# Kernel optimization log

Hardware: AMD Instinct MI355X
Metric: run time of the kernel (lower is better)

Reference implementation:

```python
import jax, jax.numpy as jnp
import numpy as np

B, L, C, H, K = 4096, 64, 7, 32, 2  # batch, series length, input ch, hidden ch, RK4 substeps per knot


def _linear_params(k, out_d, in_d):
    bound = 1.0 / np.sqrt(in_d)
    kw, kb = jax.random.split(k)
    W = jax.random.uniform(kw, (out_d, in_d), minval=-bound, maxval=bound, dtype=jnp.float32)
    b = jax.random.uniform(kb, (out_d,), minval=-bound, maxval=bound, dtype=jnp.float32)
    return W, b


def setup_inputs() -> dict:
    key = jax.random.key(0)
    ks = jax.random.split(key, 6)
    cde_src = jax.random.normal(ks[0], (B, L, C), dtype=jnp.float32)
    W_init, b_init = _linear_params(ks[1], H, C)          # initial: Linear(C, H)
    Wf1, bf1 = _linear_params(ks[2], 32, H)               # func.linear1: Linear(H, 32)
    Wf2, bf2 = _linear_params(ks[3], C * H, 32)           # func.linear2: Linear(32, C*H)
    Wo1, bo1 = _linear_params(ks[4], 16, H)               # linear1: Linear(H, 16)
    Wo2, bo2 = _linear_params(ks[5], 3, 16)               # linear2: Linear(16, 3)
    return {"cde_src": cde_src, "W_init": W_init, "b_init": b_init,
            "Wf1": Wf1, "bf1": bf1, "Wf2": Wf2, "bf2": bf2,
            "Wo1": Wo1, "bo1": bo1, "Wo2": Wo2, "bo2": bo2}


def reference(cde_src, W_init, b_init, Wf1, bf1, Wf2, bf2, Wo1, bo1, Wo2, bo2):
    x = cde_src  # (B, L, C); uniform times t = 0..L-1 (torchcde default), so dt = 1
    # Hermite cubic coefficients with backward differences (torchcde), dt = 1:
    diffs = x[:, 1:] - x[:, :-1]                       # (B, L-1, C) backward differences
    d = jnp.concatenate([diffs[:, :1], diffs], axis=1)  # derivative at each knot
    m0, m1 = d[:, :-1], d[:, 1:]
    cb = m0                                            # 'b' coeff (= dX/dt at left knot)
    two_c = 2.0 * (3.0 * diffs - 2.0 * m0 - m1)        # (B, L-1, C)
    three_d = 3.0 * (-2.0 * diffs + m0 + m1)           # (B, L-1, C)

    z0 = x[:, 0] @ W_init.T + b_init                   # initial(X(t0))  -> (B, H)

    def dXdt(t):
        idx = jnp.clip(jnp.floor(t), 0, L - 2).astype(jnp.int32)
        f = t - idx.astype(t.dtype)
        return cb[:, idx] + (two_c[:, idx] + three_d[:, idx] * f) * f  # (B, C)

    def vf(t, z):
        h1 = jax.nn.softplus(z @ Wf1.T + bf1)                    # (B, 32)
        g = jnp.tanh(h1 @ Wf2.T + bf2).reshape(z.shape[0], H, C)  # (B, H, C)
        return jnp.einsum('bhc,bc->bh', g, dXdt(t))

    h = 1.0 / K
    times = jnp.arange((L - 1) * K, dtype=jnp.float32) * h

    def step(z, t):
        k1 = vf(t, z)
        k2 = vf(t + 0.5 * h, z + (0.5 * h) * k1)
        k3 = vf(t + 0.5 * h, z + (0.5 * h) * k2)
        k4 = vf(t + h, z + h * k3)
        return z + (h / 6.0) * (k1 + 2.0 * k2 + 2.0 * k3 + k4), None

    zT, _ = jax.lax.scan(step, z0, times)  # z at final time (== zT[:, 1] in torch)
    out = jax.nn.softplus(zT @ Wo1.T + bo1) @ Wo2.T + bo2  # (B, 3)
    return out
```

## Files before the change

### kernel.cpp

```cpp
#include <hip/hip_runtime.h>
#include <hip/hip_bf16.h>
#include <stdint.h>

typedef __bf16 bf16_t;
typedef __bf16 bf16x8 __attribute__((ext_vector_type(8)));
typedef float f32x4 __attribute__((ext_vector_type(4)));

#define LOG2E 1.44269504088896340736f
#define LN2 0.69314718055994530942f

__device__ __forceinline__ float fast_exp2(float x) { return __builtin_amdgcn_exp2f(x); }
__device__ __forceinline__ float fast_log2(float x) { return __builtin_amdgcn_logf(x); }
__device__ __forceinline__ float fast_rcp(float x) { return __builtin_amdgcn_rcpf(x); }

__device__ __forceinline__ float softplus_t(float t) {
    float sp = LN2 * fast_log2(1.0f + fast_exp2(t));
    return (t > 28.9f) ? t * LN2 : sp;
}
__device__ __forceinline__ float tanh_t(float t) {
    float e = fast_exp2(t);
    return 1.0f - 2.0f * fast_rcp(1.0f + e);
}

__device__ __forceinline__ uint32_t cvt_bf16(float a) {
    uint32_t r;
    asm("v_cvt_pk_bf16_f32 %0, %1, %2" : "=v"(r) : "v"(a), "v"(a));
    return r;
}
__device__ __forceinline__ void store_hl(float v, uint16_t* ph, uint16_t* pl) {
    uint32_t h = cvt_bf16(v);
    float hf = __builtin_bit_cast(float, h << 16);
    uint32_t lo = cvt_bf16(v - hf);
    *ph = (uint16_t)h;
    *pl = (uint16_t)lo;
}

__device__ __forceinline__ float swz16(float v) {
    int r = __builtin_amdgcn_ds_swizzle(__builtin_bit_cast(int, v), 0x401F);
    return __builtin_bit_cast(float, r);
}

__global__ __launch_bounds__(512, 2) void cde_kernel(
    const float* __restrict__ x,
    const float* __restrict__ Wi,
    const float* __restrict__ bi,
    const float* __restrict__ W1,
    const float* __restrict__ b1,
    const float* __restrict__ W2,
    const float* __restrict__ b2,
    const float* __restrict__ Wo1,
    const float* __restrict__ bo1,
    const float* __restrict__ Wo2,
    const float* __restrict__ bo2,
    float* __restrict__ out)
{
    __shared__ float diffs[16][441];
    __shared__ alignas(16) float dxA[16][12];
    __shared__ alignas(16) float dxB[16][12];
    __shared__ alignas(16) uint16_t zth[16][40], ztl[16][40];
    __shared__ alignas(16) uint16_t hth[16][40], htl[16][40];
    __shared__ float zfin[16][32];
    __shared__ float wo1t[32][16];
    __shared__ float ubuf[16][16];

    const int tid = threadIdx.x;
    const int l = tid & 63;
    const int w = tid >> 6;
    const int r0 = blockIdx.x * 16;

    const int ar = l & 15;
    const int q = l >> 4;

    const int T1 = w & 1;
    const int rw = w >> 1;
    const int i1 = 16 * T1 + 4 * q + rw;

    const int h2a = 4 * w + (q >> 1);
    const int h2b = h2a + 2;

    const int bdx = 2 * w + (l >> 5);
    const int cdx = l & 31;
    const bool dxact = cdx < 7;

    bf16x8 a1h, a1l;
    {
        const float* p = &W1[(16 * T1 + ar) * 32 + 8 * q];
#pragma unroll
        for (int j = 0; j < 8; ++j) {
            float v = p[j] * LOG2E;
            bf16_t hh = (bf16_t)v;
            a1h[j] = hh;
            a1l[j] = (bf16_t)(v - (float)hh);
        }
    }
    f32x4 b1v;
#pragma unroll
    for (int r = 0; r < 4; ++r) b1v[r] = b1[16 * T1 + 4 * q + r] * LOG2E;

    bf16x8 a2h[2], a2l[2];
    f32x4 b2v[2];
#pragma unroll
    for (int t = 0; t < 2; ++t) {
        const int T = 2 * w + t;
        const int hh2 = 2 * T + (ar >> 3);
        const int cc = ar & 7;
        if (cc < 7) {
            const float* p = &W2[(hh2 * 7 + cc) * 32 + 8 * q];
#pragma unroll
            for (int j = 0; j < 8; ++j) {
                float v = p[j] * (2.0f * LOG2E);
                bf16_t hv = (bf16_t)v;
                a2h[t][j] = hv;
                a2l[t][j] = (bf16_t)(v - (float)hv);
            }
        } else {
#pragma unroll
            for (int j = 0; j < 8; ++j) { a2h[t][j] = (bf16_t)0.0f; a2l[t][j] = (bf16_t)0.0f; }
        }
#pragma unroll
        for (int r = 0; r < 4; ++r) {
            int c = 4 * (q & 1) + r;
            int hq = 2 * T + (q >> 1);
            b2v[t][r] = (c < 7) ? b2[hq * 7 + c] * (2.0f * LOG2E) : 0.0f;
        }
    }

    const bf16x8* pZh = (const bf16x8*)&zth[ar][8 * q];
    const bf16x8* pZl = (const bf16x8*)&ztl[ar][8 * q];
    const bf16x8* pHh = (const bf16x8*)&hth[ar][8 * q];
    const bf16x8* pHl = (const bf16x8*)&htl[ar][8 * q];
    const f32x4* pDxA = (const f32x4*)&dxA[ar][4 * (q & 1)];
    const f32x4* pDxB = (const f32x4*)&dxB[ar][4 * (q & 1)];
    uint16_t* pWh = &hth[ar][i1];
    uint16_t* pWl = &htl[ar][i1];
    uint16_t* pZah = &zth[ar][h2a];
    uint16_t* pZal = &ztl[ar][h2a];
    uint16_t* pZbh = &zth[ar][h2b];
    uint16_t* pZbl = &ztl[ar][h2b];

    for (int e = tid; e < 16 * 441; e += 512) {
        int r = e / 441, rem = e - r * 441;
        const float* px = &x[(size_t)(r0 + r) * 448];
        diffs[r][rem] = px[rem + 7] - px[rem];
    }
    if (tid < 16) { dxA[tid][7] = 0.0f; dxB[tid][7] = 0.0f; }
    if (dxact) {
        const float* px = &x[(size_t)(r0 + bdx) * 448];
        dxA[bdx][cdx] = px[cdx + 7] - px[cdx];
    }
    float zb0, zb1, ka0 = 0.0f, ka1 = 0.0f;
    {
        const float* px = &x[(size_t)(r0 + ar) * 448];
        float a0 = bi[h2a], a1 = bi[h2b];
#pragma unroll
        for (int c = 0; c < 7; ++c) {
            a0 += px[c] * Wi[h2a * 7 + c];
            a1 += px[c] * Wi[h2b * 7 + c];
        }
        zb0 = a0; zb1 = a1;
        store_hl(zb0, pZah, pZal);
        store_hl(zb1, pZbh, pZbl);
    }
    __syncthreads();

    const f32x4 zero4 = {0.0f, 0.0f, 0.0f, 0.0f};

    for (int k = 0; k < 126; ++k) {
#pragma unroll
        for (int s = 0; s < 4; ++s) {
            {
                bf16x8 bzh = *pZh;
                bf16x8 bzl = *pZl;
                f32x4 m1 = __builtin_amdgcn_mfma_f32_16x16x32_bf16(a1h, bzh, b1v, 0, 0, 0);
                f32x4 m2 = __builtin_amdgcn_mfma_f32_16x16x32_bf16(a1h, bzl, zero4, 0, 0, 0);
                f32x4 m3 = __builtin_amdgcn_mfma_f32_16x16x32_bf16(a1l, bzh, zero4, 0, 0, 0);
                float X;
                if (rw == 0)      X = m1[0] + m2[0] + m3[0];
                else if (rw == 1) X = m1[1] + m2[1] + m3[1];
                else if (rw == 2) X = m1[2] + m2[2] + m3[2];
                else              X = m1[3] + m2[3] + m3[3];
                store_hl(softplus_t(X), pWh, pWl);
            }
            if ((s == 0 || s == 1) && dxact) {
                int m = 2 * k + 1 + s;
                int i = m >> 2; if (i > 62) i = 62;
                float f = 0.25f * (float)(m - 4 * i);
                float D = diffs[bdx][i * 7 + cdx];
                float a = diffs[bdx][(i > 0 ? i - 1 : 0) * 7 + cdx];
                float val = a + (D - a) * (f * (4.0f - 3.0f * f));
                if (s == 0) dxB[bdx][cdx] = val;
                else        dxA[bdx][cdx] = val;
            }
            __syncthreads();

            {
                bf16x8 bhh = *pHh;
                bf16x8 bhl = *pHl;
                f32x4 dxv = (s == 0 || s == 3) ? *pDxA : *pDxB;
                float ks0, ks1;
#pragma unroll
                for (int t = 0; t < 2; ++t) {
                    f32x4 n1 = __builtin_amdgcn_mfma_f32_16x16x32_bf16(a2h[t], bhh, b2v[t], 0, 0, 0);
                    f32x4 n2 = __builtin_amdgcn_mfma_f32_16x16x32_bf16(a2h[t], bhl, zero4, 0, 0, 0);
                    f32x4 n3 = __builtin_amdgcn_mfma_f32_16x16x32_bf16(a2l[t], bhh, zero4, 0, 0, 0);
                    float pk = 0.0f;
#pragma unroll
                    for (int r = 0; r < 4; ++r)
                        pk += tanh_t(n1[r] + n2[r] + n3[r]) * dxv[r];
                    float kst = pk + swz16(pk);
                    if (t == 0) ks0 = kst; else ks1 = kst;
                }
                float zs0, zs1;
                if (s == 0) {
                    ka0 = ks0; ka1 = ks1;
                    zs0 = zb0 + 0.25f * ks0; zs1 = zb1 + 0.25f * ks1;
                } else if (s == 1) {
                    ka0 += 2.0f * ks0; ka1 += 2.0f * ks1;
                    zs0 = zb0 + 0.25f * ks0; zs1 = zb1 + 0.25f * ks1;
                } else if (s == 2) {
                    ka0 += 2.0f * ks0; ka1 += 2.0f * ks1;
                    zs0 = zb0 + 0.5f * ks0; zs1 = zb1 + 0.5f * ks1;
                } else {
                    zb0 += (1.0f / 12.0f) * (ka0 + ks0);
                    zb1 += (1.0f / 12.0f) * (ka1 + ks1);
                    zs0 = zb0; zs1 = zb1;
                }
                store_hl(zs0, pZah, pZal);
                store_hl(zs1, pZbh, pZbl);
            }
            __syncthreads();
        }
    }

    zfin[ar][h2a] = zb0;
    zfin[ar][h2b] = zb1;
    {
        int hh = tid >> 4, jj = tid & 15;
        wo1t[hh][jj] = Wo1[jj * 32 + hh];
    }
    __syncthreads();
    if (tid < 256) {
        int r = tid >> 4, jj = tid & 15;
        float acc = bo1[jj];
#pragma unroll
        for (int hh = 0; hh < 32; ++hh) acc += zfin[r][hh] * wo1t[hh][jj];
        ubuf[r][jj] = softplus_t(acc * LOG2E);
    }
    __syncthreads();
    if (tid < 48) {
        int r = tid / 3, o = tid - (tid / 3) * 3;
        float acc = bo2[o];
#pragma unroll
        for (int j = 0; j < 16; ++j) acc += ubuf[r][j] * Wo2[o * 16 + j];
        out[(size_t)(r0 + r) * 3 + o] = acc;
    }
}

extern "C" void kernel_launch(void* const* d_in, const int* in_sizes, int n_in,
                              void* d_out, int out_size, void* d_ws, size_t ws_size,
                              hipStream_t stream) {
    (void)in_sizes; (void)n_in; (void)d_ws; (void)ws_size; (void)out_size;
    const float* x   = (const float*)d_in[0];
    const float* Wi  = (const float*)d_in[1];
    const float* bi  = (const float*)d_in[2];
    const float* W1  = (const float*)d_in[3];
    const float* b1  = (const float*)d_in[4];
    const float* W2  = (const float*)d_in[5];
    const float* b2  = (const float*)d_in[6];
    const float* Wo1 = (const float*)d_in[7];
    const float* bo1 = (const float*)d_in[8];
    const float* Wo2 = (const float*)d_in[9];
    const float* bo2 = (const float*)d_in[10];
    cde_kernel<<<dim3(256), dim3(512), 0, stream>>>(x, Wi, bi, W1, b1, W2, b2,
                                                    Wo1, bo1, Wo2, bo2, (float*)d_out);
}
```

Baseline: 446.0 us.

## Halve rows per block to 8 with 4 waves and repartition MFMA work

Each block now handles 8 batch rows with 256 threads (4 waves), launching 512 blocks instead of 256 blocks of 512 threads. Each wave computes four second-layer MFMA tiles instead of two, and the 16-wide MFMA B operand is padded with zero rows for the unused half. The shared-memory z/h staging is re-laid out per wave-quadrant with packed bf16 hi/lo conversion of two values at once. The intent is more blocks across CUs and cheaper barriers with fewer waves, at the cost of wasting half of each MFMA on padding rows.

```diff
diff --git a/kernel.cpp b/kernel.cpp
--- a/kernel.cpp
+++ b/kernel.cpp
@@ -22,17 +22,10 @@
     return 1.0f - 2.0f * fast_rcp(1.0f + e);
 }
 
-__device__ __forceinline__ uint32_t cvt_bf16(float a) {
+__device__ __forceinline__ uint32_t cvt_pk(float a, float b) {
     uint32_t r;
-    asm("v_cvt_pk_bf16_f32 %0, %1, %2" : "=v"(r) : "v"(a), "v"(a));
+    asm("v_cvt_pk_bf16_f32 %0, %1, %2" : "=v"(r) : "v"(a), "v"(b));
     return r;
-}
-__device__ __forceinline__ void store_hl(float v, uint16_t* ph, uint16_t* pl) {
-    uint32_t h = cvt_bf16(v);
-    float hf = __builtin_bit_cast(float, h << 16);
-    uint32_t lo = cvt_bf16(v - hf);
-    *ph = (uint16_t)h;
-    *pl = (uint16_t)lo;
 }
 
 __device__ __forceinline__ float swz16(float v) {
@@ -40,7 +33,7 @@
     return __builtin_bit_cast(float, r);
 }
 
-__global__ __launch_bounds__(512, 2) void cde_kernel(
+__global__ __launch_bounds__(256, 2) void cde_kernel(
     const float* __restrict__ x,
     const float* __restrict__ Wi,
     const float* __restrict__ bi,
@@ -54,28 +47,28 @@
     const float* __restrict__ bo2,
     float* __restrict__ out)
 {
-    __shared__ float diffs[16][441];
+    __shared__ float diffs[8][441];
     __shared__ alignas(16) float dxA[16][12];
     __shared__ alignas(16) float dxB[16][12];
-    __shared__ alignas(16) uint16_t zth[16][40], ztl[16][40];
-    __shared__ alignas(16) uint16_t hth[16][40], htl[16][40];
+    __shared__ alignas(16) uint16_t zhS[4][16][8], zlS[4][16][8];
+    __shared__ alignas(16) uint16_t hhS[4][16][8], hlS[4][16][8];
     __shared__ float zfin[16][32];
     __shared__ float wo1t[32][16];
-    __shared__ float ubuf[16][16];
+    __shared__ float ubuf[8][16];
 
     const int tid = threadIdx.x;
     const int l = tid & 63;
     const int w = tid >> 6;
-    const int r0 = blockIdx.x * 16;
+    const int r0 = blockIdx.x * 8;
 
     const int ar = l & 15;
     const int q = l >> 4;
-
-    const int T1 = w & 1;
-    const int rw = w >> 1;
-    const int i1 = 16 * T1 + 4 * q + rw;
-
-    const int h2a = 4 * w + (q >> 1);
+    const int qlo = q & 1, qhi = q >> 1;
+    const bool brow = ar < 8;
+
+    const int T1 = w & 1, rp = w >> 1;
+
+    const int h2a = 8 * w + 4 * qlo + qhi;
     const int h2b = h2a + 2;
 
     const int bdx = 2 * w + (l >> 5);
@@ -97,15 +90,15 @@
 #pragma unroll
     for (int r = 0; r < 4; ++r) b1v[r] = b1[16 * T1 + 4 * q + r] * LOG2E;
 
-    bf16x8 a2h[2], a2l[2];
-    f32x4 b2v[2];
-#pragma unroll
-    for (int t = 0; t < 2; ++t) {
-        const int T = 2 * w + t;
-        const int hh2 = 2 * T + (ar >> 3);
+    bf16x8 a2h[4], a2l[4];
+    f32x4 b2v[4];
+#pragma unroll
+    for (int t = 0; t < 4; ++t) {
+        const int T = 4 * w + t;
+        const int hrow = 2 * T + (ar >> 3);
         const int cc = ar & 7;
         if (cc < 7) {
-            const float* p = &W2[(hh2 * 7 + cc) * 32 + 8 * q];
+            const float* p = &W2[(hrow * 7 + cc) * 32 + 8 * q];
 #pragma unroll
             for (int j = 0; j < 8; ++j) {
                 float v = p[j] * (2.0f * LOG2E);
@@ -119,37 +112,41 @@
         }
 #pragma unroll
         for (int r = 0; r < 4; ++r) {
-            int c = 4 * (q & 1) + r;
-            int hq = 2 * T + (q >> 1);
+            int c = 4 * qlo + r;
+            int hq = 2 * T + qhi;
             b2v[t][r] = (c < 7) ? b2[hq * 7 + c] * (2.0f * LOG2E) : 0.0f;
         }
     }
 
-    const bf16x8* pZh = (const bf16x8*)&zth[ar][8 * q];
-    const bf16x8* pZl = (const bf16x8*)&ztl[ar][8 * q];
-    const bf16x8* pHh = (const bf16x8*)&hth[ar][8 * q];
-    const bf16x8* pHl = (const bf16x8*)&htl[ar][8 * q];
-    const f32x4* pDxA = (const f32x4*)&dxA[ar][4 * (q & 1)];
-    const f32x4* pDxB = (const f32x4*)&dxB[ar][4 * (q & 1)];
-    uint16_t* pWh = &hth[ar][i1];
-    uint16_t* pWl = &htl[ar][i1];
-    uint16_t* pZah = &zth[ar][h2a];
-    uint16_t* pZal = &ztl[ar][h2a];
-    uint16_t* pZbh = &zth[ar][h2b];
-    uint16_t* pZbl = &ztl[ar][h2b];
-
-    for (int e = tid; e < 16 * 441; e += 512) {
+    const bf16x8* pZh = (const bf16x8*)&zhS[q][ar][0];
+    const bf16x8* pZl = (const bf16x8*)&zlS[q][ar][0];
+    const bf16x8* pHh = (const bf16x8*)&hhS[q][ar][0];
+    const bf16x8* pHl = (const bf16x8*)&hlS[q][ar][0];
+    const f32x4* pDxA = (const f32x4*)&dxA[ar][4 * qlo];
+    const f32x4* pDxB = (const f32x4*)&dxB[ar][4 * qlo];
+    uint32_t* pWh = (uint32_t*)&hhS[2 * T1 + qhi][ar][4 * qlo + 2 * rp];
+    uint32_t* pWl = (uint32_t*)&hlS[2 * T1 + qhi][ar][4 * qlo + 2 * rp];
+    uint16_t* pZ0h = &zhS[w][ar][4 * qlo + qhi];
+    uint16_t* pZ0l = &zlS[w][ar][4 * qlo + qhi];
+    uint16_t* pZ1h = &zhS[w][ar][4 * qlo + qhi + 2];
+    uint16_t* pZ1l = &zlS[w][ar][4 * qlo + qhi + 2];
+
+    ((uint32_t*)zhS)[tid] = 0;
+    ((uint32_t*)zlS)[tid] = 0;
+    ((uint32_t*)hhS)[tid] = 0;
+    ((uint32_t*)hlS)[tid] = 0;
+    if (tid < 192) { ((float*)dxA)[tid] = 0.0f; ((float*)dxB)[tid] = 0.0f; }
+    for (int e = tid; e < 8 * 441; e += 256) {
         int r = e / 441, rem = e - r * 441;
         const float* px = &x[(size_t)(r0 + r) * 448];
         diffs[r][rem] = px[rem + 7] - px[rem];
     }
-    if (tid < 16) { dxA[tid][7] = 0.0f; dxB[tid][7] = 0.0f; }
-    if (dxact) {
-        const float* px = &x[(size_t)(r0 + bdx) * 448];
-        dxA[bdx][cdx] = px[cdx + 7] - px[cdx];
-    }
-    float zb0, zb1, ka0 = 0.0f, ka1 = 0.0f;
-    {
+    for (int e = tid; e < 512; e += 256)
+        wo1t[e >> 4][e & 15] = Wo1[(e & 15) * 32 + (e >> 4)];
+    __syncthreads();
+
+    float zb0 = 0.0f, zb1 = 0.0f, ka0 = 0.0f, ka1 = 0.0f;
+    if (brow) {
         const float* px = &x[(size_t)(r0 + ar) * 448];
         float a0 = bi[h2a], a1 = bi[h2b];
 #pragma unroll
@@ -158,9 +155,16 @@
             a1 += px[c] * Wi[h2b * 7 + c];
         }
         zb0 = a0; zb1 = a1;
-        store_hl(zb0, pZah, pZal);
-        store_hl(zb1, pZbh, pZbl);
-    }
+    }
+    {
+        uint32_t rh = cvt_pk(zb0, zb1);
+        float f0 = __builtin_bit_cast(float, rh << 16);
+        float f1 = __builtin_bit_cast(float, rh & 0xffff0000u);
+        uint32_t rl = cvt_pk(zb0 - f0, zb1 - f1);
+        *pZ0h = (uint16_t)rh; *pZ1h = (uint16_t)(rh >> 16);
+        *pZ0l = (uint16_t)rl; *pZ1l = (uint16_t)(rl >> 16);
+    }
+    if (dxact) dxA[bdx][cdx] = diffs[bdx][cdx];
     __syncthreads();
 
     const f32x4 zero4 = {0.0f, 0.0f, 0.0f, 0.0f};
@@ -174,12 +178,17 @@
                 f32x4 m1 = __builtin_amdgcn_mfma_f32_16x16x32_bf16(a1h, bzh, b1v, 0, 0, 0);
                 f32x4 m2 = __builtin_amdgcn_mfma_f32_16x16x32_bf16(a1h, bzl, zero4, 0, 0, 0);
                 f32x4 m3 = __builtin_amdgcn_mfma_f32_16x16x32_bf16(a1l, bzh, zero4, 0, 0, 0);
-                float X;
-                if (rw == 0)      X = m1[0] + m2[0] + m3[0];
-                else if (rw == 1) X = m1[1] + m2[1] + m3[1];
-                else if (rw == 2) X = m1[2] + m2[2] + m3[2];
-                else              X = m1[3] + m2[3] + m3[3];
-                store_hl(softplus_t(X), pWh, pWl);
+                f32x4 S = m1 + m2 + m3;
+                float Xa = rp ? S[2] : S[0];
+                float Xb = rp ? S[3] : S[1];
+                float spa = softplus_t(Xa);
+                float spb = softplus_t(Xb);
+                uint32_t rh = cvt_pk(spa, spb);
+                float f0 = __builtin_bit_cast(float, rh << 16);
+                float f1 = __builtin_bit_cast(float, rh & 0xffff0000u);
+                uint32_t rl = cvt_pk(spa - f0, spb - f1);
+                *pWh = rh;
+                *pWl = rl;
             }
             if ((s == 0 || s == 1) && dxact) {
                 int m = 2 * k + 1 + s;
@@ -197,36 +206,42 @@
                 bf16x8 bhh = *pHh;
                 bf16x8 bhl = *pHl;
                 f32x4 dxv = (s == 0 || s == 3) ? *pDxA : *pDxB;
-                float ks0, ks1;
-#pragma unroll
-                for (int t = 0; t < 2; ++t) {
+                float ks0, ks1, ks2, ks3;
+#pragma unroll
+                for (int t = 0; t < 4; ++t) {
                     f32x4 n1 = __builtin_amdgcn_mfma_f32_16x16x32_bf16(a2h[t], bhh, b2v[t], 0, 0, 0);
                     f32x4 n2 = __builtin_amdgcn_mfma_f32_16x16x32_bf16(a2h[t], bhl, zero4, 0, 0, 0);
                     f32x4 n3 = __builtin_amdgcn_mfma_f32_16x16x32_bf16(a2l[t], bhh, zero4, 0, 0, 0);
-                    float pk = 0.0f;
-#pragma unroll
-                    for (int r = 0; r < 4; ++r)
-                        pk += tanh_t(n1[r] + n2[r] + n3[r]) * dxv[r];
+                    f32x4 S2 = n1 + n2 + n3;
+                    float pk = tanh_t(S2[0]) * dxv[0] + tanh_t(S2[1]) * dxv[1]
+                             + tanh_t(S2[2]) * dxv[2] + tanh_t(S2[3]) * dxv[3];
                     float kst = pk + swz16(pk);
-                    if (t == 0) ks0 = kst; else ks1 = kst;
+                    if (t == 0) ks0 = kst; else if (t == 1) ks1 = kst;
+                    else if (t == 2) ks2 = kst; else ks3 = kst;
                 }
+                float kd0 = qlo ? ks2 : ks0;
+                float kd1 = qlo ? ks3 : ks1;
                 float zs0, zs1;
                 if (s == 0) {
-                    ka0 = ks0; ka1 = ks1;
-                    zs0 = zb0 + 0.25f * ks0; zs1 = zb1 + 0.25f * ks1;
+                    ka0 = kd0; ka1 = kd1;
+                    zs0 = zb0 + 0.25f * kd0; zs1 = zb1 + 0.25f * kd1;
                 } else if (s == 1) {
-                    ka0 += 2.0f * ks0; ka1 += 2.0f * ks1;
-                    zs0 = zb0 + 0.25f * ks0; zs1 = zb1 + 0.25f * ks1;
+                    ka0 += 2.0f * kd0; ka1 += 2.0f * kd1;
+                    zs0 = zb0 + 0.25f * kd0; zs1 = zb1 + 0.25f * kd1;
                 } else if (s == 2) {
-                    ka0 += 2.0f * ks0; ka1 += 2.0f * ks1;
-                    zs0 = zb0 + 0.5f * ks0; zs1 = zb1 + 0.5f * ks1;
+                    ka0 += 2.0f * kd0; ka1 += 2.0f * kd1;
+                    zs0 = zb0 + 0.5f * kd0; zs1 = zb1 + 0.5f * kd1;
                 } else {
-                    zb0 += (1.0f / 12.0f) * (ka0 + ks0);
-                    zb1 += (1.0f / 12.0f) * (ka1 + ks1);
+                    zb0 += (1.0f / 12.0f) * (ka0 + kd0);
+                    zb1 += (1.0f / 12.0f) * (ka1 + kd1);
                     zs0 = zb0; zs1 = zb1;
                 }
-                store_hl(zs0, pZah, pZal);
-                store_hl(zs1, pZbh, pZbl);
+                uint32_t rh = cvt_pk(zs0, zs1);
+                float f0 = __builtin_bit_cast(float, rh << 16);
+                float f1 = __builtin_bit_cast(float, rh & 0xffff0000u);
+                uint32_t rl = cvt_pk(zs0 - f0, zs1 - f1);
+                *pZ0h = (uint16_t)rh; *pZ1h = (uint16_t)(rh >> 16);
+                *pZ0l = (uint16_t)rl; *pZ1l = (uint16_t)(rl >> 16);
             }
             __syncthreads();
         }
@@ -234,12 +249,8 @@
 
     zfin[ar][h2a] = zb0;
     zfin[ar][h2b] = zb1;
-    {
-        int hh = tid >> 4, jj = tid & 15;
-        wo1t[hh][jj] = Wo1[jj * 32 + hh];
-    }
-    __syncthreads();
-    if (tid < 256) {
+    __syncthreads();
+    if (tid < 128) {
         int r = tid >> 4, jj = tid & 15;
         float acc = bo1[jj];
 #pragma unroll
@@ -247,8 +258,8 @@
         ubuf[r][jj] = softplus_t(acc * LOG2E);
     }
     __syncthreads();
-    if (tid < 48) {
-        int r = tid / 3, o = tid - (tid / 3) * 3;
+    if (tid < 24) {
+        int r = tid / 3, o = tid - 3 * (tid / 3);
         float acc = bo2[o];
 #pragma unroll
         for (int j = 0; j < 16; ++j) acc += ubuf[r][j] * Wo2[o * 16 + j];
@@ -271,6 +282,6 @@
     const float* bo1 = (const float*)d_in[8];
     const float* Wo2 = (const float*)d_in[9];
     const float* bo2 = (const float*)d_in[10];
-    cde_kernel<<<dim3(256), dim3(512), 0, stream>>>(x, Wi, bi, W1, b1, W2, b2,
+    cde_kernel<<<dim3(512), dim3(256), 0, stream>>>(x, Wi, bi, W1, b1, W2, b2,
                                                     Wo1, bo1, Wo2, bo2, (float*)d_out);
 }
```

Result: slower. 594.7 us (+33.3%).
